# Kernel tuning notes

Hardware: AMD Instinct MI355X
Metric: run time of the kernel (lower is better)

The kernel has to match this reference:

```python
import jax, jax.numpy as jnp
import numpy as np

B, S, T = 4, 1024, 2048
HID = 1024
NH = 16
NKV = 4
HD = HID // NH  # 64


def setup_inputs() -> dict:
    key = jax.random.key(0)
    ks = jax.random.split(key, 6)
    scale = 1.0 / np.sqrt(HID)
    return {
        "x": jax.random.normal(ks[0], (B, S, HID), dtype=jnp.float32),
        "context": jax.random.normal(ks[1], (B, T, HID), dtype=jnp.float32),
        "Wq": jax.random.normal(ks[2], (NH * HD, HID), dtype=jnp.float32) * scale,
        "Wk": jax.random.normal(ks[3], (NKV * HD, HID), dtype=jnp.float32) * scale,
        "Wv": jax.random.normal(ks[4], (NKV * HD, HID), dtype=jnp.float32) * scale,
        "Wo": jax.random.normal(ks[5], (HID, NH * HD), dtype=jnp.float32) * scale,
    }


def reference(x, context, Wq, Wk, Wv, Wo):
    Bx, Sx, _ = x.shape
    Tx = context.shape[1]
    rep = NH // NKV
    # projections (Linear with no bias: y = x @ W.T)
    q = (x @ Wq.T).reshape(Bx, Sx, NKV, rep, HD)          # group query heads by KV head
    k = (context @ Wk.T).reshape(Bx, Tx, NKV, HD)
    v = (context @ Wv.T).reshape(Bx, Tx, NKV, HD)
    scale = 1.0 / jnp.sqrt(jnp.asarray(HD, dtype=q.dtype))
    # scores: [B, NKV, rep, S, T] -- shares K across the rep grouped heads
    # (math-identical to repeat_interleave then SDPA, without materializing K/V copies)
    scores = jnp.einsum("bsgrd,btgd->bgrst", q, k) * scale
    attn = jax.nn.softmax(scores, axis=-1)
    out = jnp.einsum("bgrst,btgd->bsgrd", attn, v)        # [B,S,NKV,rep,HD]
    out = out.reshape(Bx, Sx, NH * HD)
    return out @ Wo.T
```

## Files before the change

kernel.cpp:

```cpp
#include <hip/hip_runtime.h>
#include <hip/hip_bf16.h>
#include <stdint.h>

typedef __bf16 bf16x8 __attribute__((ext_vector_type(8)));
typedef float f32x4 __attribute__((ext_vector_type(4)));
typedef unsigned short u16;
typedef unsigned int u32;

struct __align__(8) us4 { u16 x, y, z, w; };
struct __align__(16) us8 { u16 v[8]; };

#define LOG2E 1.44269504088896f

__device__ __forceinline__ void async_load16(const void* g, void* l) {
    __builtin_amdgcn_global_load_lds(
        (const __attribute__((address_space(1))) u32*)(uintptr_t)g,
        (__attribute__((address_space(3))) u32*)(u32)(uintptr_t)l,
        16, 0, 0);
}

__device__ __forceinline__ u16 f2bfbits(float f) {
    __bf16 h = (__bf16)f;
    return __builtin_bit_cast(u16, h);
}

__global__ __launch_bounds__(256) void convert_all(
    const float* __restrict__ x, const float* __restrict__ ctx,
    const float* __restrict__ wq, const float* __restrict__ wk,
    const float* __restrict__ wv, const float* __restrict__ wo,
    u16* __restrict__ xb, u16* __restrict__ ctxb, u16* __restrict__ wqb,
    u16* __restrict__ wkb, u16* __restrict__ wvb, u16* __restrict__ wob) {
    int i = blockIdx.x * 256 + threadIdx.x;
    const float* s; u16* d; int j;
    if (i < 524288)        { s = x;   d = xb;   j = i; }
    else if (i < 1572864)  { s = ctx; d = ctxb; j = i - 524288; }
    else if (i < 1703936)  { s = wq;  d = wqb;  j = i - 1572864; }
    else if (i < 1736704)  { s = wk;  d = wkb;  j = i - 1703936; }
    else if (i < 1769472)  { s = wv;  d = wvb;  j = i - 1736704; }
    else                   { s = wo;  d = wob;  j = i - 1769472; }
    const float4* sp = (const float4*)s + (size_t)j * 2;
    float4 a = sp[0], b = sp[1];
    us8 o;
    o.v[0] = f2bfbits(a.x); o.v[1] = f2bfbits(a.y);
    o.v[2] = f2bfbits(a.z); o.v[3] = f2bfbits(a.w);
    o.v[4] = f2bfbits(b.x); o.v[5] = f2bfbits(b.y);
    o.v[6] = f2bfbits(b.z); o.v[7] = f2bfbits(b.w);
    *(us8*)(d + (size_t)j * 8) = o;
}

template <int MODE, int OUTF32>
__global__ __launch_bounds__(256) void gemm_bt(const u16* __restrict__ A,
                                               const u16* __restrict__ B0,
                                               const u16* __restrict__ B1,
                                               void* __restrict__ C0,
                                               void* __restrict__ C1,
                                               int M, int N, int K, float alpha) {
    __shared__ u16 As[128 * 64];
    __shared__ u16 Bs[128 * 64];
    const int tid = threadIdx.x;
    const int w = tid >> 6, lane = tid & 63, quad = lane >> 4, id = lane & 15;
    const int mtile = blockIdx.y * 128, ntile = blockIdx.x * 128;
    const int wr = (w >> 1) * 64, wc = (w & 1) * 64;
    const int lrow = lane >> 3, lcol = (lane & 7) * 8;
    const u16* Bm = (MODE == 3 && blockIdx.z) ? B1 : B0;

    f32x4 acc[4][4];
#pragma unroll
    for (int i = 0; i < 4; i++)
#pragma unroll
        for (int j = 0; j < 4; j++) acc[i][j] = (f32x4){0.f, 0.f, 0.f, 0.f};

    for (int k0 = 0; k0 < K; k0 += 64) {
        __syncthreads();
#pragma unroll
        for (int is = 0; is < 4; is++) {
            int r = is * 32 + w * 8 + lrow;
            async_load16(A + (size_t)(mtile + r) * K + k0 + lcol, &As[(is * 32 + w * 8) * 64]);
        }
#pragma unroll
        for (int is = 0; is < 4; is++) {
            int r = is * 32 + w * 8 + lrow;
            async_load16(Bm + (size_t)(ntile + r) * K + k0 + lcol, &Bs[(is * 32 + w * 8) * 64]);
        }
        __syncthreads();
#pragma unroll
        for (int kk = 0; kk < 2; kk++) {
            bf16x8 af[4], bfr[4];
#pragma unroll
            for (int i = 0; i < 4; i++)
                af[i] = *(const bf16x8*)&As[(wr + i * 16 + id) * 64 + kk * 32 + quad * 8];
#pragma unroll
            for (int j = 0; j < 4; j++)
                bfr[j] = *(const bf16x8*)&Bs[(wc + j * 16 + id) * 64 + kk * 32 + quad * 8];
#pragma unroll
            for (int i = 0; i < 4; i++)
#pragma unroll
                for (int j = 0; j < 4; j++)
                    acc[i][j] = __builtin_amdgcn_mfma_f32_16x16x32_bf16(af[i], bfr[j], acc[i][j], 0, 0, 0);
        }
    }

#pragma unroll
    for (int i = 0; i < 4; i++)
#pragma unroll
        for (int j = 0; j < 4; j++) {
            int mbase = mtile + wr + i * 16 + quad * 4;
            int n = ntile + wc + j * 16 + id;
            if (MODE == 3 && blockIdx.z == 1) {
                u16* C = (u16*)C1;
                int b = mbase >> 11, t = mbase & 2047;
                int g = n >> 6, d = n & 63;
                us4 pk;
                pk.x = f2bfbits(acc[i][j][0]);
                pk.y = f2bfbits(acc[i][j][1]);
                pk.z = f2bfbits(acc[i][j][2]);
                pk.w = f2bfbits(acc[i][j][3]);
                *(us4*)&C[((size_t)((b << 2) + g) * 64 + d) * 2048 + t] = pk;
            } else {
#pragma unroll
                for (int r = 0; r < 4; r++) {
                    int m = mbase + r;
                    float v = acc[i][j][r];
                    if (MODE == 0) {
                        v *= alpha;
                        size_t addr = (size_t)m * N + n;
                        if (OUTF32) ((float*)C0)[addr] = v;
                        else        ((u16*)C0)[addr] = f2bfbits(v);
                    } else {
                        int b = m >> 11, t = m & 2047;
                        int g = n >> 6, d = n & 63;
                        ((u16*)C0)[((size_t)((b << 2) + g) * 2048 + t) * 64 + d] = f2bfbits(v);
                    }
                }
            }
        }
}

__global__ __launch_bounds__(256) void attn_kernel(const u16* __restrict__ q,
                                                   const u16* __restrict__ k2,
                                                   const u16* __restrict__ vT,
                                                   u16* __restrict__ o) {
    __shared__ u16 Ks[64 * 64];
    __shared__ u16 Vt[64 * 64];
    __shared__ u16 Ps[4 * 32 * 72];
    const int tid = threadIdx.x;
    const int w = tid >> 6, lane = tid & 63, quad = lane >> 4, id = lane & 15;
    const int b = blockIdx.z, h = blockIdx.y, g = h >> 2;
    const int s0 = blockIdx.x * 128;
    const int stgswz = (((lane & 7) ^ (lane >> 3)) * 8);
    const int rdsw = id & 7;

    bf16x8 qf[2][2];
#pragma unroll
    for (int rb = 0; rb < 2; rb++) {
        const size_t base = ((size_t)(b * 1024 + s0 + w * 32 + rb * 16 + id)) * 1024 + h * 64;
        qf[rb][0] = *(const bf16x8*)&q[base + quad * 8];
        qf[rb][1] = *(const bf16x8*)&q[base + 32 + quad * 8];
    }
    f32x4 acc[2][4];
    float lpart[2][4];
#pragma unroll
    for (int rb = 0; rb < 2; rb++)
#pragma unroll
        for (int i = 0; i < 4; i++) {
            acc[rb][i] = (f32x4){0.f, 0.f, 0.f, 0.f};
            lpart[rb][i] = 0.f;
        }

    const size_t kbase = ((size_t)(b * 4 + g)) * 2048 * 64;
    const size_t vbase = ((size_t)(b * 4 + g)) * 64 * 2048;
    const int pbase = w * 2304;

    for (int t0 = 0; t0 < 2048; t0 += 64) {
        __syncthreads();
#pragma unroll
        for (int is = 0; is < 2; is++) {
            int tl = is * 32 + w * 8;
            async_load16(&k2[kbase + (size_t)(t0 + tl + (lane >> 3)) * 64 + stgswz],
                         &Ks[tl * 64]);
        }
#pragma unroll
        for (int is = 0; is < 2; is++) {
            int dl = is * 32 + w * 8;
            async_load16(&vT[vbase + (size_t)(dl + (lane >> 3)) * 2048 + t0 + stgswz],
                         &Vt[dl * 64]);
        }
        __syncthreads();

        f32x4 s[2][4];
#pragma unroll
        for (int rb = 0; rb < 2; rb++)
#pragma unroll
            for (int cb = 0; cb < 4; cb++) s[rb][cb] = (f32x4){0.f, 0.f, 0.f, 0.f};
#pragma unroll
        for (int kk = 0; kk < 2; kk++)
#pragma unroll
            for (int cb = 0; cb < 4; cb++) {
                bf16x8 kf = *(const bf16x8*)&Ks[(cb * 16 + id) * 64 + (((kk * 4 + quad) ^ rdsw) * 8)];
                s[0][cb] = __builtin_amdgcn_mfma_f32_16x16x32_bf16(qf[0][kk], kf, s[0][cb], 0, 0, 0);
                s[1][cb] = __builtin_amdgcn_mfma_f32_16x16x32_bf16(qf[1][kk], kf, s[1][cb], 0, 0, 0);
            }

#pragma unroll
        for (int rb = 0; rb < 2; rb++)
#pragma unroll
            for (int cb = 0; cb < 4; cb++)
#pragma unroll
                for (int r = 0; r < 4; r++) {
                    float pv = __builtin_exp2f(s[rb][cb][r] * LOG2E);
                    lpart[rb][r] += pv;
                    Ps[pbase + (rb * 16 + quad * 4 + r) * 72 + cb * 16 + id] = f2bfbits(pv);
                }

#pragma unroll
        for (int kk = 0; kk < 2; kk++) {
            bf16x8 pf0 = *(const bf16x8*)&Ps[pbase + id * 72 + kk * 32 + quad * 8];
            bf16x8 pf1 = *(const bf16x8*)&Ps[pbase + (16 + id) * 72 + kk * 32 + quad * 8];
#pragma unroll
            for (int db = 0; db < 4; db++) {
                bf16x8 vf = *(const bf16x8*)&Vt[(db * 16 + id) * 64 + (((kk * 4 + quad) ^ rdsw) * 8)];
                acc[0][db] = __builtin_amdgcn_mfma_f32_16x16x32_bf16(pf0, vf, acc[0][db], 0, 0, 0);
                acc[1][db] = __builtin_amdgcn_mfma_f32_16x16x32_bf16(pf1, vf, acc[1][db], 0, 0, 0);
            }
        }
    }

    float inv[2][4];
#pragma unroll
    for (int rb = 0; rb < 2; rb++)
#pragma unroll
        for (int r = 0; r < 4; r++) {
            float l = lpart[rb][r];
#pragma unroll
            for (int off = 1; off < 16; off <<= 1) l += __shfl_xor(l, off);
            inv[rb][r] = 1.0f / l;
        }
#pragma unroll
    for (int rb = 0; rb < 2; rb++)
#pragma unroll
        for (int db = 0; db < 4; db++)
#pragma unroll
            for (int r = 0; r < 4; r++) {
                int srow = s0 + w * 32 + rb * 16 + quad * 4 + r;
                o[((size_t)(b * 1024 + srow)) * 1024 + h * 64 + db * 16 + id] =
                    f2bfbits(acc[rb][db][r] * inv[rb][r]);
            }
}

extern "C" void kernel_launch(void* const* d_in, const int* in_sizes, int n_in,
                              void* d_out, int out_size, void* d_ws, size_t ws_size,
                              hipStream_t stream) {
    (void)in_sizes; (void)n_in; (void)out_size; (void)ws_size;
    const float* x   = (const float*)d_in[0];
    const float* ctx = (const float*)d_in[1];
    const float* Wq  = (const float*)d_in[2];
    const float* Wk  = (const float*)d_in[3];
    const float* Wv  = (const float*)d_in[4];
    const float* Wo  = (const float*)d_in[5];
    float* out = (float*)d_out;

    u16* xb   = (u16*)d_ws;
    u16* ctxb = xb   + 4096 * 1024;
    u16* Wqb  = ctxb + 4 * 2048 * 1024;
    u16* Wkb  = Wqb  + 1024 * 1024;
    u16* Wvb  = Wkb  + 256 * 1024;
    u16* Wob  = Wvb  + 256 * 1024;
    u16* q    = Wob  + 1024 * 1024;
    u16* k2   = q    + 4096 * 1024;
    u16* vT   = k2   + 4 * 4 * 2048 * 64;
    u16* o    = vT   + 4 * 4 * 64 * 2048;

    convert_all<<<7424, 256, 0, stream>>>(x, ctx, Wq, Wk, Wv, Wo,
                                          xb, ctxb, Wqb, Wkb, Wvb, Wob);

    gemm_bt<0, 0><<<dim3(8, 32), 256, 0, stream>>>(xb, Wqb, nullptr, q, nullptr,
                                                   4096, 1024, 1024, 0.125f);
    gemm_bt<3, 0><<<dim3(2, 64, 2), 256, 0, stream>>>(ctxb, Wkb, Wvb, k2, vT,
                                                      8192, 256, 1024, 1.0f);
    attn_kernel<<<dim3(8, 16, 4), 256, 0, stream>>>(q, k2, vT, o);
    gemm_bt<0, 1><<<dim3(8, 32), 256, 0, stream>>>(o, Wob, nullptr, out, nullptr,
                                                   4096, 1024, 1024, 1.0f);
}
```

Baseline: 253.0 us.

## Fuse QKV projections, double-buffer attention K/V, compute row sums via MFMA

Merges the Q and K/V projection GEMMs into one 512-block launch and folds log2e into the Q scale so the softmax exp2 needs no multiply. The attention kernel gains double-buffered K/V LDS staging with one barrier per tile, an XCD-aware block remap so blocks sharing a KV head land on the same die, and an MFMA against a ones vector in place of scalar row-sum accumulation and shuffles. These changes target launch overhead, load latency, barrier count and VALU work, at the cost of more LDS per block and extra MFMA issue. Softmax still has no max subtraction, same as before.

```diff
diff --git a/kernel.cpp b/kernel.cpp
--- a/kernel.cpp
+++ b/kernel.cpp
@@ -11,6 +11,7 @@
 struct __align__(16) us8 { u16 v[8]; };
 
 #define LOG2E 1.44269504088896f
+#define QSCALE (0.125f * LOG2E)
 
 __device__ __forceinline__ void async_load16(const void* g, void* l) {
     __builtin_amdgcn_global_load_lds(
@@ -48,13 +49,100 @@
     *(us8*)(d + (size_t)j * 8) = o;
 }
 
-template <int MODE, int OUTF32>
-__global__ __launch_bounds__(256) void gemm_bt(const u16* __restrict__ A,
-                                               const u16* __restrict__ B0,
-                                               const u16* __restrict__ B1,
-                                               void* __restrict__ C0,
-                                               void* __restrict__ C1,
-                                               int M, int N, int K, float alpha) {
+__global__ __launch_bounds__(256) void proj_qkv(
+    const u16* __restrict__ xb, const u16* __restrict__ ctxb,
+    const u16* __restrict__ Wqb, const u16* __restrict__ Wkb,
+    const u16* __restrict__ Wvb,
+    u16* __restrict__ q, u16* __restrict__ k2, u16* __restrict__ vT) {
+    __shared__ u16 As[128 * 64];
+    __shared__ u16 Bs[128 * 64];
+    const int tid = threadIdx.x;
+    const int w = tid >> 6, lane = tid & 63, quad = lane >> 4, id = lane & 15;
+    const int wr = (w >> 1) * 64, wc = (w & 1) * 64;
+    const int lrow = lane >> 3, lcol = (lane & 7) * 8;
+
+    const int bid = blockIdx.x;
+    const u16 *A, *Bm;
+    int mtile, ntile, mode;
+    if (bid < 256) {
+        mode = 0; A = xb; Bm = Wqb;
+        mtile = (bid >> 3) * 128; ntile = (bid & 7) * 128;
+    } else {
+        int t = bid - 256, z = t >> 7, r = t & 127;
+        mode = 1 + z; A = ctxb; Bm = z ? Wvb : Wkb;
+        mtile = (r >> 1) * 128; ntile = (r & 1) * 128;
+    }
+
+    f32x4 acc[4][4];
+#pragma unroll
+    for (int i = 0; i < 4; i++)
+#pragma unroll
+        for (int j = 0; j < 4; j++) acc[i][j] = (f32x4){0.f, 0.f, 0.f, 0.f};
+
+    for (int k0 = 0; k0 < 1024; k0 += 64) {
+        __syncthreads();
+#pragma unroll
+        for (int is = 0; is < 4; is++) {
+            int r = is * 32 + w * 8 + lrow;
+            async_load16(A + (size_t)(mtile + r) * 1024 + k0 + lcol, &As[(is * 32 + w * 8) * 64]);
+        }
+#pragma unroll
+        for (int is = 0; is < 4; is++) {
+            int r = is * 32 + w * 8 + lrow;
+            async_load16(Bm + (size_t)(ntile + r) * 1024 + k0 + lcol, &Bs[(is * 32 + w * 8) * 64]);
+        }
+        __syncthreads();
+#pragma unroll
+        for (int kk = 0; kk < 2; kk++) {
+            bf16x8 af[4], bfr[4];
+#pragma unroll
+            for (int i = 0; i < 4; i++)
+                af[i] = *(const bf16x8*)&As[(wr + i * 16 + id) * 64 + kk * 32 + quad * 8];
+#pragma unroll
+            for (int j = 0; j < 4; j++)
+                bfr[j] = *(const bf16x8*)&Bs[(wc + j * 16 + id) * 64 + kk * 32 + quad * 8];
+#pragma unroll
+            for (int i = 0; i < 4; i++)
+#pragma unroll
+                for (int j = 0; j < 4; j++)
+                    acc[i][j] = __builtin_amdgcn_mfma_f32_16x16x32_bf16(af[i], bfr[j], acc[i][j], 0, 0, 0);
+        }
+    }
+
+#pragma unroll
+    for (int i = 0; i < 4; i++)
+#pragma unroll
+        for (int j = 0; j < 4; j++) {
+            int mbase = mtile + wr + i * 16 + quad * 4;
+            int n = ntile + wc + j * 16 + id;
+            if (mode == 2) {
+                int b = mbase >> 11, t = mbase & 2047;
+                int g = n >> 6, d = n & 63;
+                us4 pk;
+                pk.x = f2bfbits(acc[i][j][0]);
+                pk.y = f2bfbits(acc[i][j][1]);
+                pk.z = f2bfbits(acc[i][j][2]);
+                pk.w = f2bfbits(acc[i][j][3]);
+                *(us4*)&vT[((size_t)((b << 2) + g) * 64 + d) * 2048 + t] = pk;
+            } else if (mode == 1) {
+#pragma unroll
+                for (int r = 0; r < 4; r++) {
+                    int m = mbase + r;
+                    int b = m >> 11, t = m & 2047;
+                    int g = n >> 6, d = n & 63;
+                    k2[((size_t)((b << 2) + g) * 2048 + t) * 64 + d] = f2bfbits(acc[i][j][r]);
+                }
+            } else {
+#pragma unroll
+                for (int r = 0; r < 4; r++)
+                    q[(size_t)(mbase + r) * 1024 + n] = f2bfbits(acc[i][j][r] * QSCALE);
+            }
+        }
+}
+
+__global__ __launch_bounds__(256) void gemm_out(const u16* __restrict__ A,
+                                                const u16* __restrict__ Bm,
+                                                float* __restrict__ C) {
     __shared__ u16 As[128 * 64];
     __shared__ u16 Bs[128 * 64];
     const int tid = threadIdx.x;
@@ -62,7 +150,6 @@
     const int mtile = blockIdx.y * 128, ntile = blockIdx.x * 128;
     const int wr = (w >> 1) * 64, wc = (w & 1) * 64;
     const int lrow = lane >> 3, lcol = (lane & 7) * 8;
-    const u16* Bm = (MODE == 3 && blockIdx.z) ? B1 : B0;
 
     f32x4 acc[4][4];
 #pragma unroll
@@ -70,17 +157,17 @@
 #pragma unroll
         for (int j = 0; j < 4; j++) acc[i][j] = (f32x4){0.f, 0.f, 0.f, 0.f};
 
-    for (int k0 = 0; k0 < K; k0 += 64) {
+    for (int k0 = 0; k0 < 1024; k0 += 64) {
         __syncthreads();
 #pragma unroll
         for (int is = 0; is < 4; is++) {
             int r = is * 32 + w * 8 + lrow;
-            async_load16(A + (size_t)(mtile + r) * K + k0 + lcol, &As[(is * 32 + w * 8) * 64]);
+            async_load16(A + (size_t)(mtile + r) * 1024 + k0 + lcol, &As[(is * 32 + w * 8) * 64]);
         }
 #pragma unroll
         for (int is = 0; is < 4; is++) {
             int r = is * 32 + w * 8 + lrow;
-            async_load16(Bm + (size_t)(ntile + r) * K + k0 + lcol, &Bs[(is * 32 + w * 8) * 64]);
+            async_load16(Bm + (size_t)(ntile + r) * 1024 + k0 + lcol, &Bs[(is * 32 + w * 8) * 64]);
         }
         __syncthreads();
 #pragma unroll
@@ -106,33 +193,9 @@
         for (int j = 0; j < 4; j++) {
             int mbase = mtile + wr + i * 16 + quad * 4;
             int n = ntile + wc + j * 16 + id;
-            if (MODE == 3 && blockIdx.z == 1) {
-                u16* C = (u16*)C1;
-                int b = mbase >> 11, t = mbase & 2047;
-                int g = n >> 6, d = n & 63;
-                us4 pk;
-                pk.x = f2bfbits(acc[i][j][0]);
-                pk.y = f2bfbits(acc[i][j][1]);
-                pk.z = f2bfbits(acc[i][j][2]);
-                pk.w = f2bfbits(acc[i][j][3]);
-                *(us4*)&C[((size_t)((b << 2) + g) * 64 + d) * 2048 + t] = pk;
-            } else {
-#pragma unroll
-                for (int r = 0; r < 4; r++) {
-                    int m = mbase + r;
-                    float v = acc[i][j][r];
-                    if (MODE == 0) {
-                        v *= alpha;
-                        size_t addr = (size_t)m * N + n;
-                        if (OUTF32) ((float*)C0)[addr] = v;
-                        else        ((u16*)C0)[addr] = f2bfbits(v);
-                    } else {
-                        int b = m >> 11, t = m & 2047;
-                        int g = n >> 6, d = n & 63;
-                        ((u16*)C0)[((size_t)((b << 2) + g) * 2048 + t) * 64 + d] = f2bfbits(v);
-                    }
-                }
-            }
+#pragma unroll
+            for (int r = 0; r < 4; r++)
+                C[(size_t)(mbase + r) * 1024 + n] = acc[i][j][r];
         }
 }
 
@@ -140,13 +203,20 @@
                                                    const u16* __restrict__ k2,
                                                    const u16* __restrict__ vT,
                                                    u16* __restrict__ o) {
-    __shared__ u16 Ks[64 * 64];
-    __shared__ u16 Vt[64 * 64];
+    __shared__ u16 Ks[2][64 * 64];
+    __shared__ u16 Vt[2][64 * 64];
     __shared__ u16 Ps[4 * 32 * 72];
     const int tid = threadIdx.x;
     const int w = tid >> 6, lane = tid & 63, quad = lane >> 4, id = lane & 15;
-    const int b = blockIdx.z, h = blockIdx.y, g = h >> 2;
-    const int s0 = blockIdx.x * 128;
+
+    const int bid = blockIdx.x;
+    const int xcd = bid & 7, slot = bid >> 3;
+    const int bg = xcd * 2 + (slot >> 5);
+    const int inner = slot & 31;
+    const int b = bg >> 2, g = bg & 3;
+    const int h = g * 4 + (inner >> 3);
+    const int s0 = (inner & 7) * 128;
+
     const int stgswz = (((lane & 7) ^ (lane >> 3)) * 8);
     const int rdsw = id & 7;
 
@@ -157,35 +227,47 @@
         qf[rb][0] = *(const bf16x8*)&q[base + quad * 8];
         qf[rb][1] = *(const bf16x8*)&q[base + 32 + quad * 8];
     }
-    f32x4 acc[2][4];
-    float lpart[2][4];
-#pragma unroll
-    for (int rb = 0; rb < 2; rb++)
-#pragma unroll
-        for (int i = 0; i < 4; i++) {
-            acc[rb][i] = (f32x4){0.f, 0.f, 0.f, 0.f};
-            lpart[rb][i] = 0.f;
-        }
+
+    bf16x8 ones;
+    {
+        __bf16 one = (__bf16)1.0f;
+#pragma unroll
+        for (int i = 0; i < 8; i++) ones[i] = one;
+    }
+
+    f32x4 acc[2][4], accl[2];
+#pragma unroll
+    for (int rb = 0; rb < 2; rb++) {
+        accl[rb] = (f32x4){0.f, 0.f, 0.f, 0.f};
+#pragma unroll
+        for (int i = 0; i < 4; i++) acc[rb][i] = (f32x4){0.f, 0.f, 0.f, 0.f};
+    }
 
     const size_t kbase = ((size_t)(b * 4 + g)) * 2048 * 64;
     const size_t vbase = ((size_t)(b * 4 + g)) * 64 * 2048;
     const int pbase = w * 2304;
 
-    for (int t0 = 0; t0 < 2048; t0 += 64) {
-        __syncthreads();
+    auto stage = [&](int t0, int buf) {
 #pragma unroll
         for (int is = 0; is < 2; is++) {
             int tl = is * 32 + w * 8;
             async_load16(&k2[kbase + (size_t)(t0 + tl + (lane >> 3)) * 64 + stgswz],
-                         &Ks[tl * 64]);
+                         &Ks[buf][tl * 64]);
         }
 #pragma unroll
         for (int is = 0; is < 2; is++) {
             int dl = is * 32 + w * 8;
             async_load16(&vT[vbase + (size_t)(dl + (lane >> 3)) * 2048 + t0 + stgswz],
-                         &Vt[dl * 64]);
-        }
-        __syncthreads();
+                         &Vt[buf][dl * 64]);
+        }
+    };
+
+    stage(0, 0);
+    __syncthreads();
+
+    int cur = 0;
+    for (int t0 = 0; t0 < 2048; t0 += 64) {
+        if (t0 + 64 < 2048) stage(t0 + 64, cur ^ 1);
 
         f32x4 s[2][4];
 #pragma unroll
@@ -196,7 +278,7 @@
         for (int kk = 0; kk < 2; kk++)
 #pragma unroll
             for (int cb = 0; cb < 4; cb++) {
-                bf16x8 kf = *(const bf16x8*)&Ks[(cb * 16 + id) * 64 + (((kk * 4 + quad) ^ rdsw) * 8)];
+                bf16x8 kf = *(const bf16x8*)&Ks[cur][(cb * 16 + id) * 64 + (((kk * 4 + quad) ^ rdsw) * 8)];
                 s[0][cb] = __builtin_amdgcn_mfma_f32_16x16x32_bf16(qf[0][kk], kf, s[0][cb], 0, 0, 0);
                 s[1][cb] = __builtin_amdgcn_mfma_f32_16x16x32_bf16(qf[1][kk], kf, s[1][cb], 0, 0, 0);
             }
@@ -206,45 +288,42 @@
 #pragma unroll
             for (int cb = 0; cb < 4; cb++)
 #pragma unroll
-                for (int r = 0; r < 4; r++) {
-                    float pv = __builtin_exp2f(s[rb][cb][r] * LOG2E);
-                    lpart[rb][r] += pv;
-                    Ps[pbase + (rb * 16 + quad * 4 + r) * 72 + cb * 16 + id] = f2bfbits(pv);
-                }
+                for (int r = 0; r < 4; r++)
+                    Ps[pbase + (rb * 16 + quad * 4 + r) * 72 + cb * 16 + id] =
+                        f2bfbits(__builtin_exp2f(s[rb][cb][r]));
 
 #pragma unroll
         for (int kk = 0; kk < 2; kk++) {
             bf16x8 pf0 = *(const bf16x8*)&Ps[pbase + id * 72 + kk * 32 + quad * 8];
             bf16x8 pf1 = *(const bf16x8*)&Ps[pbase + (16 + id) * 72 + kk * 32 + quad * 8];
+            accl[0] = __builtin_amdgcn_mfma_f32_16x16x32_bf16(pf0, ones, accl[0], 0, 0, 0);
+            accl[1] = __builtin_amdgcn_mfma_f32_16x16x32_bf16(pf1, ones, accl[1], 0, 0, 0);
 #pragma unroll
             for (int db = 0; db < 4; db++) {
-                bf16x8 vf = *(const bf16x8*)&Vt[(db * 16 + id) * 64 + (((kk * 4 + quad) ^ rdsw) * 8)];
+                bf16x8 vf = *(const bf16x8*)&Vt[cur][(db * 16 + id) * 64 + (((kk * 4 + quad) ^ rdsw) * 8)];
                 acc[0][db] = __builtin_amdgcn_mfma_f32_16x16x32_bf16(pf0, vf, acc[0][db], 0, 0, 0);
                 acc[1][db] = __builtin_amdgcn_mfma_f32_16x16x32_bf16(pf1, vf, acc[1][db], 0, 0, 0);
             }
         }
-    }
-
-    float inv[2][4];
-#pragma unroll
-    for (int rb = 0; rb < 2; rb++)
-#pragma unroll
-        for (int r = 0; r < 4; r++) {
-            float l = lpart[rb][r];
-#pragma unroll
-            for (int off = 1; off < 16; off <<= 1) l += __shfl_xor(l, off);
-            inv[rb][r] = 1.0f / l;
-        }
-#pragma unroll
-    for (int rb = 0; rb < 2; rb++)
+
+        __syncthreads();
+        cur ^= 1;
+    }
+
+#pragma unroll
+    for (int rb = 0; rb < 2; rb++) {
+        f32x4 inv;
+#pragma unroll
+        for (int r = 0; r < 4; r++) inv[r] = 1.0f / accl[rb][r];
 #pragma unroll
         for (int db = 0; db < 4; db++)
 #pragma unroll
             for (int r = 0; r < 4; r++) {
                 int srow = s0 + w * 32 + rb * 16 + quad * 4 + r;
                 o[((size_t)(b * 1024 + srow)) * 1024 + h * 64 + db * 16 + id] =
-                    f2bfbits(acc[rb][db][r] * inv[rb][r]);
+                    f2bfbits(acc[rb][db][r] * inv[r]);
             }
+    }
 }
 
 extern "C" void kernel_launch(void* const* d_in, const int* in_sizes, int n_in,
@@ -272,12 +351,7 @@
 
     convert_all<<<7424, 256, 0, stream>>>(x, ctx, Wq, Wk, Wv, Wo,
                                           xb, ctxb, Wqb, Wkb, Wvb, Wob);
-
-    gemm_bt<0, 0><<<dim3(8, 32), 256, 0, stream>>>(xb, Wqb, nullptr, q, nullptr,
-                                                   4096, 1024, 1024, 0.125f);
-    gemm_bt<3, 0><<<dim3(2, 64, 2), 256, 0, stream>>>(ctxb, Wkb, Wvb, k2, vT,
-                                                      8192, 256, 1024, 1.0f);
-    attn_kernel<<<dim3(8, 16, 4), 256, 0, stream>>>(q, k2, vT, o);
-    gemm_bt<0, 1><<<dim3(8, 32), 256, 0, stream>>>(o, Wob, nullptr, out, nullptr,
-                                                   4096, 1024, 1024, 1.0f);
-}
+    proj_qkv<<<512, 256, 0, stream>>>(xb, ctxb, Wqb, Wkb, Wvb, q, k2, vT);
+    attn_kernel<<<512, 256, 0, stream>>>(q, k2, vT, o);
+    gemm_out<<<dim3(8, 32), 256, 0, stream>>>(o, Wob, out);
+}
```

After: 225.1 us. -11.0%, faster.
